# Kernel optimization log

Measured on AMD Instinct MI355X. Metric: run time of the kernel, lower is better.

Reference implementation:

```python
import jax, jax.numpy as jnp
import numpy as np

BS = 4
EMBED = 256
HEADS = 8
LEVELS = 4
POINTS = 4
HD = EMBED // HEADS  # 32
SHAPES = np.array([[96, 96], [48, 48], [24, 24], [12, 12]], dtype=np.int64)
LQ = int((SHAPES[:, 0] * SHAPES[:, 1]).sum())  # 12240


def _offset_bias():
    # faithful to MSDeformableAttention._reset_parameters grid init
    thetas = np.arange(HEADS, dtype=np.float32) * (2.0 * np.pi / HEADS)
    g = np.stack([np.cos(thetas), np.sin(thetas)], -1)
    g = g / np.abs(g).max(-1, keepdims=True)
    g = np.tile(g.reshape(HEADS, 1, 1, 2), (1, LEVELS, POINTS, 1))
    g = g * np.arange(1, POINTS + 1, dtype=np.float32).reshape(1, 1, -1, 1)
    return jnp.asarray(g.reshape(-1), dtype=jnp.float32)


def setup_inputs() -> dict:
    key = jax.random.key(0)
    ks = jax.random.split(key, 8)
    tp = HEADS * LEVELS * POINTS
    d = {}
    d["query"] = jax.random.normal(ks[0], (BS, LQ, EMBED), jnp.float32)
    d["reference_points"] = jax.random.uniform(ks[1], (BS, LQ, LEVELS, 2), jnp.float32)
    d["value"] = jax.random.normal(ks[2], (BS, LQ, EMBED), jnp.float32)
    d["value_spatial_shapes"] = SHAPES  # static numpy, int
    d["W_off"] = jax.random.normal(ks[3], (EMBED, tp * 2), jnp.float32) * 0.01
    d["b_off"] = _offset_bias()
    d["W_attn"] = jax.random.normal(ks[4], (EMBED, tp), jnp.float32) * 0.02
    d["b_attn"] = jnp.zeros((tp,), jnp.float32)
    d["W_val"] = jax.random.normal(ks[5], (EMBED, EMBED), jnp.float32) * (1.0 / np.sqrt(EMBED).astype(np.float32))
    d["b_val"] = jnp.zeros((EMBED,), jnp.float32)
    d["W_out"] = jax.random.normal(ks[6], (EMBED, EMBED), jnp.float32) * (1.0 / np.sqrt(EMBED).astype(np.float32))
    d["b_out"] = jnp.zeros((EMBED,), jnp.float32)
    return d


def _bilinear_sample(img, grid):
    # img: [B,H,W,C]; grid: [B,Q,P,2] in [-1,1] (x,y)
    # matches F.grid_sample(mode='bilinear', padding_mode='zeros', align_corners=False)
    B, H, W, C = img.shape
    gx = (grid[..., 0] + 1.0) * (W * 0.5) - 0.5
    gy = (grid[..., 1] + 1.0) * (H * 0.5) - 0.5
    x0 = jnp.floor(gx)
    y0 = jnp.floor(gy)
    wx = gx - x0
    wy = gy - y0
    x0i = x0.astype(jnp.int32)
    y0i = y0.astype(jnp.int32)
    x1i = x0i + 1
    y1i = y0i + 1
    flat = img.reshape(B, H * W, C)

    def corner(xi, yi, w):
        valid = (xi >= 0) & (xi < W) & (yi >= 0) & (yi < H)
        idx = jnp.clip(yi, 0, H - 1) * W + jnp.clip(xi, 0, W - 1)
        v = jnp.take_along_axis(flat, idx.reshape(B, -1, 1), axis=1)
        v = v.reshape(idx.shape + (C,))
        return v * (w * valid)[..., None]

    return (corner(x0i, y0i, (1.0 - wx) * (1.0 - wy))
            + corner(x1i, y0i, wx * (1.0 - wy))
            + corner(x0i, y1i, (1.0 - wx) * wy)
            + corner(x1i, y1i, wx * wy))


def reference(query, reference_points, value, value_spatial_shapes,
              W_off, b_off, W_attn, b_attn, W_val, b_val, W_out, b_out):
    shapes = np.asarray(value_spatial_shapes)  # static [L,2] (H,W)
    bs, Lq, _ = query.shape
    v = (value @ W_val + b_val).reshape(bs, -1, HEADS, HD)  # [bs,Lv,H,hd]
    off = (query @ W_off + b_off).reshape(bs, Lq, HEADS, LEVELS, POINTS, 2)
    aw = jax.nn.softmax((query @ W_attn + b_attn).reshape(bs, Lq, HEADS, LEVELS * POINTS), axis=-1)
    aw = aw.reshape(bs, Lq, HEADS, LEVELS, POINTS)
    # normalizer is (W,H) per level
    norm = jnp.asarray(shapes[:, ::-1].copy(), jnp.float32).reshape(1, 1, 1, LEVELS, 1, 2)
    loc = reference_points[:, :, None, :, None, :] + off / norm
    grids = 2.0 * loc - 1.0  # [bs,Lq,H,L,P,2]

    acc = jnp.zeros((bs * HEADS, Lq, HD), query.dtype)
    start = 0
    for lvl in range(LEVELS):
        h, w = int(shapes[lvl, 0]), int(shapes[lvl, 1])
        v_l = v[:, start:start + h * w].reshape(bs, h, w, HEADS, HD)
        v_l = v_l.transpose(0, 3, 1, 2, 4).reshape(bs * HEADS, h, w, HD)
        g_l = grids[:, :, :, lvl].transpose(0, 2, 1, 3, 4).reshape(bs * HEADS, Lq, POINTS, 2)
        s_l = _bilinear_sample(v_l, g_l)  # [bs*H, Lq, P, hd]
        w_l = aw[:, :, :, lvl].transpose(0, 2, 1, 3).reshape(bs * HEADS, Lq, POINTS)
        acc = acc + jnp.einsum('bqpc,bqp->bqc', s_l, w_l)
        start += h * w

    out = acc.reshape(bs, HEADS, Lq, HD).transpose(0, 2, 1, 3).reshape(bs, Lq, EMBED)
    return out @ W_out + b_out
```

## Files before the change

### kernel.cpp

```cpp
#include <hip/hip_runtime.h>
#include <hip/hip_bf16.h>

static constexpr int BS     = 4;
static constexpr int EMBED  = 256;
static constexpr int HEADS  = 8;
static constexpr int LEVELS = 4;
static constexpr int POINTS = 4;
static constexpr int HD     = 32;
static constexpr int LQ     = 12240;
static constexpr int NROW   = BS * LQ;
static constexpr int LVL_W[4]  = {96, 48, 24, 12};
static constexpr int LVL_H[4]  = {96, 48, 24, 12};
static constexpr int LVL_ST[4] = {0, 9216, 11520, 12096};

typedef __attribute__((ext_vector_type(8))) short short8;
typedef __attribute__((ext_vector_type(4))) float f32x4;
typedef __attribute__((ext_vector_type(2))) float f32x2;

__device__ __forceinline__ unsigned short f2bf(float f) {
    unsigned int u = __float_as_uint(f);
    unsigned int r = (u + 0x7FFFu + ((u >> 16) & 1u)) >> 16;
    return (unsigned short)r;
}
__device__ __forceinline__ float bf2f(unsigned short b) {
    return __uint_as_float(((unsigned int)b) << 16);
}

__device__ __forceinline__ void pkfma(f32x2& a, unsigned int u, f32x2 w) {
    f32x2 v;
    v.x = __uint_as_float(u << 16);
    v.y = __uint_as_float(u & 0xffff0000u);
    asm("v_pk_fma_f32 %0, %1, %2, %0" : "+v"(a) : "v"(v), "v"(w));
}

__global__ __launch_bounds__(256) void prep_weights(
    const float* __restrict__ W_off, const float* __restrict__ W_attn,
    const float* __restrict__ W_val, const float* __restrict__ W_out,
    unsigned short* __restrict__ WT_oa, unsigned short* __restrict__ WT_val,
    unsigned short* __restrict__ WT_out)
{
    const int gid = blockIdx.x * 256 + threadIdx.x;
    const int k = gid & 255;
    const int n = gid >> 8;
    if (n < 384) {
        const float v = (n < 256) ? W_off[k * 256 + n] : W_attn[k * 128 + (n - 256)];
        WT_oa[n * 256 + k] = f2bf(v);
    } else if (n < 640) {
        const int nn = n - 384;
        WT_val[nn * 256 + k] = f2bf(W_val[k * 256 + nn]);
    } else {
        const int nn = n - 640;
        WT_out[nn * 256 + k] = f2bf(W_out[k * 256 + nn]);
    }
}

template <int NTW, bool A_BF16, bool OUT_BF16>
__global__ __launch_bounds__(256) void gemm_mfma(
    const void* __restrict__ Av, const unsigned short* __restrict__ Wt,
    const float* __restrict__ bias0, const float* __restrict__ bias1, int nsplit,
    void* __restrict__ Cv, int N)
{
    constexpr int NB = NTW * 64;
    constexpr int K  = 256;
    __shared__ __align__(16) unsigned short As[64][40];
    __shared__ __align__(16) unsigned short Bs[NB][40];

    const int tid = threadIdx.x;
    const int m0 = blockIdx.y * 64;
    const int n0 = blockIdx.x * NB;
    const int w  = tid >> 6;
    const int l  = tid & 63;
    const int lm = l & 15;
    const int lq = l >> 4;

    const int sr = tid >> 2;
    const int kg = (tid & 3) * 8;

    float4 pa0, pa1; short8 pa_bf;
    short8 pb[NTW];

    auto gload = [&](int k0) {
        if (A_BF16) {
            const unsigned short* A = (const unsigned short*)Av;
            pa_bf = *(const short8*)&A[(size_t)(m0 + sr) * K + k0 + kg];
        } else {
            const float* A = (const float*)Av;
            const float* ap = &A[(size_t)(m0 + sr) * K + k0 + kg];
            pa0 = *(const float4*)ap;
            pa1 = *(const float4*)(ap + 4);
        }
        #pragma unroll
        for (int i = 0; i < NTW; ++i) {
            const int slot = tid + i * 256;
            const int n  = slot >> 2;
            const int kk = (slot & 3) * 8;
            pb[i] = *(const short8*)&Wt[(size_t)(n0 + n) * K + k0 + kk];
        }
    };

    f32x4 acc[4][NTW];
    #pragma unroll
    for (int rg = 0; rg < 4; ++rg)
        #pragma unroll
        for (int nt = 0; nt < NTW; ++nt)
            acc[rg][nt] = (f32x4){0.f, 0.f, 0.f, 0.f};

    gload(0);
    #pragma unroll 2
    for (int k0 = 0; k0 < K; k0 += 32) {
        if (A_BF16) {
            *(short8*)&As[sr][kg] = pa_bf;
        } else {
            uint4 pk;
            pk.x = (unsigned int)f2bf(pa0.x) | ((unsigned int)f2bf(pa0.y) << 16);
            pk.y = (unsigned int)f2bf(pa0.z) | ((unsigned int)f2bf(pa0.w) << 16);
            pk.z = (unsigned int)f2bf(pa1.x) | ((unsigned int)f2bf(pa1.y) << 16);
            pk.w = (unsigned int)f2bf(pa1.z) | ((unsigned int)f2bf(pa1.w) << 16);
            *(uint4*)&As[sr][kg] = pk;
        }
        #pragma unroll
        for (int i = 0; i < NTW; ++i) {
            const int slot = tid + i * 256;
            const int n  = slot >> 2;
            const int kk = (slot & 3) * 8;
            *(short8*)&Bs[n][kk] = pb[i];
        }
        __syncthreads();

        if (k0 + 32 < K) gload(k0 + 32);

        short8 af[4];
        #pragma unroll
        for (int rg = 0; rg < 4; ++rg)
            af[rg] = *(const short8*)&As[rg * 16 + lm][lq * 8];
        #pragma unroll
        for (int nt = 0; nt < NTW; ++nt) {
            const short8 bf = *(const short8*)&Bs[(w * NTW + nt) * 16 + lm][lq * 8];
            #pragma unroll
            for (int rg = 0; rg < 4; ++rg)
                acc[rg][nt] = __builtin_amdgcn_mfma_f32_16x16x32_bf16(af[rg], bf, acc[rg][nt], 0, 0, 0);
        }
        __syncthreads();
    }

    #pragma unroll
    for (int nt = 0; nt < NTW; ++nt) {
        const int col = n0 + (w * NTW + nt) * 16 + lm;
        const float b = (col < nsplit) ? bias0[col] : bias1[col - nsplit];
        #pragma unroll
        for (int rg = 0; rg < 4; ++rg)
            #pragma unroll
            for (int r = 0; r < 4; ++r) {
                const int row = m0 + rg * 16 + lq * 4 + r;
                const float v = acc[rg][nt][r] + b;
                if (OUT_BF16) ((unsigned short*)Cv)[(size_t)row * N + col] = f2bf(v);
                else          ((float*)Cv)[(size_t)row * N + col] = v;
            }
    }
}

__global__ __launch_bounds__(256) void loc_aw_kernel(
    float* __restrict__ OA, const float* __restrict__ refp)
{
    const int tid = threadIdx.x;
    const int row = blockIdx.x * 2 + (tid >> 7);
    const int t = tid & 127;
    const int l = (t >> 2) & 3;
    float* rowp = OA + (size_t)row * 384;

    float logit = rowp[256 + t];
    float m = logit;
    #pragma unroll
    for (int d = 8; d >= 1; d >>= 1) m = fmaxf(m, __shfl_xor(m, d, 16));
    float e = __expf(logit - m);
    float s = e;
    #pragma unroll
    for (int d = 8; d >= 1; d >>= 1) s += __shfl_xor(s, d, 16);
    rowp[256 + t] = e / s;

    const float ox = rowp[t * 2 + 0];
    const float oy = rowp[t * 2 + 1];
    const float rx = refp[(size_t)row * 8 + l * 2 + 0];
    const float ry = refp[(size_t)row * 8 + l * 2 + 1];
    const float Wl = (float)LVL_W[l];
    const float Hl = (float)LVL_H[l];
    const float lx = rx + ox / Wl;
    const float ly = ry + oy / Hl;
    rowp[t * 2 + 0] = lx * Wl - 0.5f;
    rowp[t * 2 + 1] = ly * Hl - 0.5f;
}

__global__ __launch_bounds__(256) void sample_kernel(
    const unsigned short* __restrict__ V,
    const float* __restrict__ OA,
    unsigned short* __restrict__ ACC)
{
    __shared__ unsigned int pr[512 * 12];

    const int tid = threadIdx.x;

    #pragma unroll
    for (int ss = 0; ss < 2; ++ss) {
        const int s  = tid + ss * 256;
        const int lp = s >> 5;
        const int r  = (s >> 3) & 3;
        const int h  = s & 7;
        const int lvl = lp >> 2;
        const int Wl = LVL_W[lvl], Hl = LVL_H[lvl], st = LVL_ST[lvl];
        const float* rowp = OA + (size_t)(blockIdx.x * 4 + r) * 384;

        const float gx  = rowp[h * 32 + lp * 2 + 0];
        const float gy  = rowp[h * 32 + lp * 2 + 1];
        const float wgt = rowp[256 + h * 16 + lp];

        const float fx = floorf(gx), fy = floorf(gy);
        const float wx = gx - fx,    wy = gy - fy;
        const int x0 = (int)fx, y0 = (int)fy;
        const int x1 = x0 + 1,  y1 = y0 + 1;

        const bool bx0 = ((unsigned)x0 < (unsigned)Wl);
        const bool bx1 = ((unsigned)x1 < (unsigned)Wl);
        const bool by0 = ((unsigned)y0 < (unsigned)Hl);
        const bool by1 = ((unsigned)y1 < (unsigned)Hl);
        const float w00 = (bx0 && by0) ? (1.f - wx) * (1.f - wy) * wgt : 0.f;
        const float w10 = (bx1 && by0) ? wx * (1.f - wy) * wgt : 0.f;
        const float w01 = (bx0 && by1) ? (1.f - wx) * wy * wgt : 0.f;
        const float w11 = (bx1 && by1) ? wx * wy * wgt : 0.f;

        const int cx0 = min(max(x0, 0), Wl - 1);
        const int cx1 = min(max(x1, 0), Wl - 1);
        const int cy0 = min(max(y0, 0), Hl - 1);
        const int cy1 = min(max(y1, 0), Hl - 1);

        unsigned int* p = &pr[s * 12];
        uint4 o;
        o.x = (unsigned int)(st + cy0 * Wl + cx0) * 512u;
        o.y = (unsigned int)(st + cy0 * Wl + cx1) * 512u;
        o.z = (unsigned int)(st + cy1 * Wl + cx0) * 512u;
        o.w = (unsigned int)(st + cy1 * Wl + cx1) * 512u;
        *(uint4*)p = o;
        uint4 wA, wB;
        wA.x = __float_as_uint(w00); wA.y = wA.x;
        wA.z = __float_as_uint(w10); wA.w = wA.z;
        wB.x = __float_as_uint(w01); wB.y = wB.x;
        wB.z = __float_as_uint(w11); wB.w = wB.z;
        *(uint4*)(p + 4) = wA;
        *(uint4*)(p + 8) = wB;
    }
    __syncthreads();

    const int w    = tid >> 6;
    const int l    = tid & 63;
    const int half = l >> 5;
    const int head = (l >> 2) & 7;
    const int c16  = (l & 3) * 16;

    const int row  = __builtin_amdgcn_readfirstlane(blockIdx.x * 4 + w);
    const int b    = row / LQ;
    const char* vrow = (const char*)V + (size_t)b * ((size_t)LQ * 512);
    const unsigned int lane_byte = (unsigned int)(head * 64 + c16);
    const int sid0 = half * 8 * 32 + w * 8 + head;

    unsigned int ofs[2][4];
    f32x2 wp[2][4];
    uint4 dat[2][4];
    f32x2 acc[4];
    #pragma unroll
    for (int i = 0; i < 4; ++i) acc[i] = (f32x2){0.f, 0.f};

    auto ldprep = [&](int j, int buf) {
        const unsigned int* p = &pr[(sid0 + j * 32) * 12];
        const uint4 o = *(const uint4*)p;
        ofs[buf][0] = o.x; ofs[buf][1] = o.y; ofs[buf][2] = o.z; ofs[buf][3] = o.w;
        #pragma unroll
        for (int c = 0; c < 4; ++c)
            wp[buf][c] = *(const f32x2*)(p + 4 + 2 * c);
    };
    auto ldval = [&](int buf) {
        #pragma unroll
        for (int c = 0; c < 4; ++c)
            dat[buf][c] = *(const uint4*)(vrow + (lane_byte + ofs[buf][c]));
    };
    auto consume = [&](int buf) {
        #pragma unroll
        for (int c = 0; c < 4; ++c) {
            const uint4 d = dat[buf][c];
            const f32x2 ww = wp[buf][c];
            pkfma(acc[0], d.x, ww);
            pkfma(acc[1], d.y, ww);
            pkfma(acc[2], d.z, ww);
            pkfma(acc[3], d.w, ww);
        }
    };

    ldprep(0, 0);
    ldval(0);
    #pragma unroll
    for (int j = 0; j < 8; ++j) {
        if (j < 7) {
            ldprep(j + 1, (j + 1) & 1);
            ldval((j + 1) & 1);
        }
        consume(j & 1);
    }

    #pragma unroll
    for (int i = 0; i < 4; ++i) {
        acc[i].x += __shfl_xor(acc[i].x, 32);
        acc[i].y += __shfl_xor(acc[i].y, 32);
    }
    if (half == 0) {
        uint4 o;
        o.x = (unsigned int)f2bf(acc[0].x) | ((unsigned int)f2bf(acc[0].y) << 16);
        o.y = (unsigned int)f2bf(acc[1].x) | ((unsigned int)f2bf(acc[1].y) << 16);
        o.z = (unsigned int)f2bf(acc[2].x) | ((unsigned int)f2bf(acc[2].y) << 16);
        o.w = (unsigned int)f2bf(acc[3].x) | ((unsigned int)f2bf(acc[3].y) << 16);
        *(uint4*)((char*)(ACC + (size_t)row * EMBED) + head * 64 + c16) = o;
    }
}

extern "C" void kernel_launch(void* const* d_in, const int* in_sizes, int n_in,
                              void* d_out, int out_size, void* d_ws, size_t ws_size,
                              hipStream_t stream) {
    const float* query  = (const float*)d_in[0];
    const float* refp   = (const float*)d_in[1];
    const float* value  = (const float*)d_in[2];
    const float* W_off  = (const float*)d_in[4];
    const float* b_off  = (const float*)d_in[5];
    const float* W_attn = (const float*)d_in[6];
    const float* b_attn = (const float*)d_in[7];
    const float* W_val  = (const float*)d_in[8];
    const float* b_val  = (const float*)d_in[9];
    const float* W_out  = (const float*)d_in[10];
    const float* b_out  = (const float*)d_in[11];
    float* out = (float*)d_out;

    unsigned short* WT_oa  = (unsigned short*)d_ws;
    unsigned short* WT_val = WT_oa  + 384 * 256;
    unsigned short* WT_out = WT_val + 256 * 256;
    unsigned short* V      = WT_out + 256 * 256;
    float*          OA     = (float*)(V + (size_t)NROW * EMBED);
    unsigned short* ACCb   = (unsigned short*)(OA + (size_t)NROW * 384);

    dim3 blk(256);

    prep_weights<<<896, blk, 0, stream>>>(W_off, W_attn, W_val, W_out,
                                          WT_oa, WT_val, WT_out);
    gemm_mfma<4, false, true><<<dim3(1, NROW / 64), blk, 0, stream>>>(
        value, WT_val, b_val, b_val, 256, V, 256);
    gemm_mfma<3, false, false><<<dim3(2, NROW / 64), blk, 0, stream>>>(
        query, WT_oa, b_off, b_attn, 256, OA, 384);
    loc_aw_kernel<<<NROW / 2, blk, 0, stream>>>(OA, refp);
    sample_kernel<<<NROW / 4, blk, 0, stream>>>(V, OA, ACCb);
    gemm_mfma<4, true, false><<<dim3(1, NROW / 64), blk, 0, stream>>>(
        ACCb, WT_out, b_out, b_out, 256, out, 256);
}
```

Baseline: 382.9 us.

## Fuse softmax and location computation into the sampling kernel

Removes the separate loc_aw kernel and computes the softmax over attention logits and the sampling coordinates inside the sampling kernel's prep phase, using shared-memory reductions. This avoids a launch and a read-modify-write pass over the 384-column OA buffer. The LDS layout is shrunk from 12 to 8 words per sample by storing four scalar weights instead of duplicated pairs. The inner loop is also restructured to pair corners for packed FMA, with a final horizontal add. The trade-off is extra syncthreads and a reduction inside the sampling kernel, plus a launch-bounds occupancy hint.

```diff
diff --git a/kernel.cpp b/kernel.cpp
--- a/kernel.cpp
+++ b/kernel.cpp
@@ -22,14 +22,8 @@
     unsigned int r = (u + 0x7FFFu + ((u >> 16) & 1u)) >> 16;
     return (unsigned short)r;
 }
-__device__ __forceinline__ float bf2f(unsigned short b) {
-    return __uint_as_float(((unsigned int)b) << 16);
-}
-
-__device__ __forceinline__ void pkfma(f32x2& a, unsigned int u, f32x2 w) {
-    f32x2 v;
-    v.x = __uint_as_float(u << 16);
-    v.y = __uint_as_float(u & 0xffff0000u);
+
+__device__ __forceinline__ void pkfma(f32x2& a, f32x2 v, f32x2 w) {
     asm("v_pk_fma_f32 %0, %1, %2, %0" : "+v"(a) : "v"(v), "v"(w));
 }
 
@@ -159,93 +153,95 @@
     }
 }
 
-__global__ __launch_bounds__(256) void loc_aw_kernel(
-    float* __restrict__ OA, const float* __restrict__ refp)
-{
-    const int tid = threadIdx.x;
-    const int row = blockIdx.x * 2 + (tid >> 7);
-    const int t = tid & 127;
-    const int l = (t >> 2) & 3;
-    float* rowp = OA + (size_t)row * 384;
-
-    float logit = rowp[256 + t];
-    float m = logit;
-    #pragma unroll
-    for (int d = 8; d >= 1; d >>= 1) m = fmaxf(m, __shfl_xor(m, d, 16));
-    float e = __expf(logit - m);
-    float s = e;
-    #pragma unroll
-    for (int d = 8; d >= 1; d >>= 1) s += __shfl_xor(s, d, 16);
-    rowp[256 + t] = e / s;
-
-    const float ox = rowp[t * 2 + 0];
-    const float oy = rowp[t * 2 + 1];
-    const float rx = refp[(size_t)row * 8 + l * 2 + 0];
-    const float ry = refp[(size_t)row * 8 + l * 2 + 1];
-    const float Wl = (float)LVL_W[l];
-    const float Hl = (float)LVL_H[l];
-    const float lx = rx + ox / Wl;
-    const float ly = ry + oy / Hl;
-    rowp[t * 2 + 0] = lx * Wl - 0.5f;
-    rowp[t * 2 + 1] = ly * Hl - 0.5f;
-}
-
-__global__ __launch_bounds__(256) void sample_kernel(
+__global__ __launch_bounds__(256, 8) void sample_kernel(
     const unsigned short* __restrict__ V,
     const float* __restrict__ OA,
+    const float* __restrict__ refp,
     unsigned short* __restrict__ ACC)
 {
-    __shared__ unsigned int pr[512 * 12];
+    __shared__ __align__(16) unsigned int pr_o[512][4];
+    __shared__ __align__(16) unsigned int pr_w[512][4];
 
     const int tid = threadIdx.x;
 
-    #pragma unroll
-    for (int ss = 0; ss < 2; ++ss) {
-        const int s  = tid + ss * 256;
-        const int lp = s >> 5;
-        const int r  = (s >> 3) & 3;
-        const int h  = s & 7;
-        const int lvl = lp >> 2;
-        const int Wl = LVL_W[lvl], Hl = LVL_H[lvl], st = LVL_ST[lvl];
-        const float* rowp = OA + (size_t)(blockIdx.x * 4 + r) * 384;
-
-        const float gx  = rowp[h * 32 + lp * 2 + 0];
-        const float gy  = rowp[h * 32 + lp * 2 + 1];
-        const float wgt = rowp[256 + h * 16 + lp];
-
-        const float fx = floorf(gx), fy = floorf(gy);
-        const float wx = gx - fx,    wy = gy - fy;
-        const int x0 = (int)fx, y0 = (int)fy;
-        const int x1 = x0 + 1,  y1 = y0 + 1;
-
-        const bool bx0 = ((unsigned)x0 < (unsigned)Wl);
-        const bool bx1 = ((unsigned)x1 < (unsigned)Wl);
-        const bool by0 = ((unsigned)y0 < (unsigned)Hl);
-        const bool by1 = ((unsigned)y1 < (unsigned)Hl);
-        const float w00 = (bx0 && by0) ? (1.f - wx) * (1.f - wy) * wgt : 0.f;
-        const float w10 = (bx1 && by0) ? wx * (1.f - wy) * wgt : 0.f;
-        const float w01 = (bx0 && by1) ? (1.f - wx) * wy * wgt : 0.f;
-        const float w11 = (bx1 && by1) ? wx * wy * wgt : 0.f;
-
-        const int cx0 = min(max(x0, 0), Wl - 1);
-        const int cx1 = min(max(x1, 0), Wl - 1);
-        const int cy0 = min(max(y0, 0), Hl - 1);
-        const int cy1 = min(max(y1, 0), Hl - 1);
-
-        unsigned int* p = &pr[s * 12];
-        uint4 o;
-        o.x = (unsigned int)(st + cy0 * Wl + cx0) * 512u;
-        o.y = (unsigned int)(st + cy0 * Wl + cx1) * 512u;
-        o.z = (unsigned int)(st + cy1 * Wl + cx0) * 512u;
-        o.w = (unsigned int)(st + cy1 * Wl + cx1) * 512u;
-        *(uint4*)p = o;
-        uint4 wA, wB;
-        wA.x = __float_as_uint(w00); wA.y = wA.x;
-        wA.z = __float_as_uint(w10); wA.w = wA.z;
-        wB.x = __float_as_uint(w01); wB.y = wB.x;
-        wB.z = __float_as_uint(w11); wB.w = wB.z;
-        *(uint4*)(p + 4) = wA;
-        *(uint4*)(p + 8) = wB;
+    {
+        const int g = tid & 31;
+        const int r = g >> 3;
+        const int h = g & 7;
+        const int L = tid >> 5;
+        const int prow = blockIdx.x * 4 + r;
+        const float* rowp = OA + (size_t)prow * 384;
+
+        const float lg0 = rowp[256 + h * 16 + L];
+        const float lg1 = rowp[256 + h * 16 + L + 8];
+
+        float* smax = (float*)pr_w;
+        float* ssum = smax + 264;
+        smax[L * 33 + g] = fmaxf(lg0, lg1);
+        __syncthreads();
+        float m = smax[g];
+        #pragma unroll
+        for (int k = 1; k < 8; ++k) m = fmaxf(m, smax[k * 33 + g]);
+        const float e0 = __expf(lg0 - m);
+        const float e1 = __expf(lg1 - m);
+        ssum[L * 33 + g] = e0 + e1;
+        __syncthreads();
+        float sden = ssum[g];
+        #pragma unroll
+        for (int k = 1; k < 8; ++k) sden += ssum[k * 33 + g];
+        const float inv = 1.0f / sden;
+
+        uint4 wstash[2];
+        int   sidx[2];
+        #pragma unroll
+        for (int ss = 0; ss < 2; ++ss) {
+            const int lp  = L + ss * 8;
+            const int s   = lp * 32 + g;
+            const int lvl = lp >> 2;
+            const int Wl = LVL_W[lvl], Hl = LVL_H[lvl], st = LVL_ST[lvl];
+
+            const float2 oxy = *(const float2*)&rowp[h * 32 + lp * 2];
+            const float2 rxy = *(const float2*)&refp[(size_t)prow * 8 + lvl * 2];
+            const float wgt = (ss ? e1 : e0) * inv;
+
+            const float gx = (rxy.x + oxy.x / (float)Wl) * (float)Wl - 0.5f;
+            const float gy = (rxy.y + oxy.y / (float)Hl) * (float)Hl - 0.5f;
+
+            const float fx = floorf(gx), fy = floorf(gy);
+            const float wx = gx - fx,    wy = gy - fy;
+            const int x0 = (int)fx, y0 = (int)fy;
+            const int x1 = x0 + 1,  y1 = y0 + 1;
+
+            const bool bx0 = ((unsigned)x0 < (unsigned)Wl);
+            const bool bx1 = ((unsigned)x1 < (unsigned)Wl);
+            const bool by0 = ((unsigned)y0 < (unsigned)Hl);
+            const bool by1 = ((unsigned)y1 < (unsigned)Hl);
+            const float w00 = (bx0 && by0) ? (1.f - wx) * (1.f - wy) * wgt : 0.f;
+            const float w10 = (bx1 && by0) ? wx * (1.f - wy) * wgt : 0.f;
+            const float w01 = (bx0 && by1) ? (1.f - wx) * wy * wgt : 0.f;
+            const float w11 = (bx1 && by1) ? wx * wy * wgt : 0.f;
+
+            const int cx0 = min(max(x0, 0), Wl - 1);
+            const int cx1 = min(max(x1, 0), Wl - 1);
+            const int cy0 = min(max(y0, 0), Hl - 1);
+            const int cy1 = min(max(y1, 0), Hl - 1);
+
+            uint4 o;
+            o.x = (unsigned int)(st + cy0 * Wl + cx0) * 512u;
+            o.y = (unsigned int)(st + cy0 * Wl + cx1) * 512u;
+            o.z = (unsigned int)(st + cy1 * Wl + cx0) * 512u;
+            o.w = (unsigned int)(st + cy1 * Wl + cx1) * 512u;
+            *(uint4*)&pr_o[s][0] = o;
+
+            uint4 wv;
+            wv.x = __float_as_uint(w00); wv.y = __float_as_uint(w10);
+            wv.z = __float_as_uint(w01); wv.w = __float_as_uint(w11);
+            wstash[ss] = wv;
+            sidx[ss] = s;
+        }
+        __syncthreads();
+        *(uint4*)&pr_w[sidx[0]][0] = wstash[0];
+        *(uint4*)&pr_w[sidx[1]][0] = wstash[1];
     }
     __syncthreads();
 
@@ -259,62 +255,67 @@
     const int b    = row / LQ;
     const char* vrow = (const char*)V + (size_t)b * ((size_t)LQ * 512);
     const unsigned int lane_byte = (unsigned int)(head * 64 + c16);
-    const int sid0 = half * 8 * 32 + w * 8 + head;
-
-    unsigned int ofs[2][4];
-    f32x2 wp[2][4];
+    const int sid0 = half * 256 + w * 8 + head;
+
     uint4 dat[2][4];
-    f32x2 acc[4];
-    #pragma unroll
-    for (int i = 0; i < 4; ++i) acc[i] = (f32x2){0.f, 0.f};
-
-    auto ldprep = [&](int j, int buf) {
-        const unsigned int* p = &pr[(sid0 + j * 32) * 12];
-        const uint4 o = *(const uint4*)p;
-        ofs[buf][0] = o.x; ofs[buf][1] = o.y; ofs[buf][2] = o.z; ofs[buf][3] = o.w;
-        #pragma unroll
-        for (int c = 0; c < 4; ++c)
-            wp[buf][c] = *(const f32x2*)(p + 4 + 2 * c);
+    f32x2 accA[4], accB[4];
+    #pragma unroll
+    for (int i = 0; i < 4; ++i) { accA[i] = (f32x2){0.f,0.f}; accB[i] = (f32x2){0.f,0.f}; }
+
+    auto ldissue = [&](int j, int buf) {
+        const uint4 o = *(const uint4*)&pr_o[sid0 + j * 32][0];
+        dat[buf][0] = *(const uint4*)(vrow + (lane_byte + o.x));
+        dat[buf][1] = *(const uint4*)(vrow + (lane_byte + o.y));
+        dat[buf][2] = *(const uint4*)(vrow + (lane_byte + o.z));
+        dat[buf][3] = *(const uint4*)(vrow + (lane_byte + o.w));
     };
-    auto ldval = [&](int buf) {
-        #pragma unroll
-        for (int c = 0; c < 4; ++c)
-            dat[buf][c] = *(const uint4*)(vrow + (lane_byte + ofs[buf][c]));
+    auto pkstep = [&](f32x2& A, f32x2& B, unsigned u0, unsigned u1, f32x2 w2) {
+        f32x2 pa, pb;
+        pa.x = __uint_as_float(u0 << 16);
+        pa.y = __uint_as_float(u1 << 16);
+        pb.x = __uint_as_float(u0 & 0xffff0000u);
+        pb.y = __uint_as_float(u1 & 0xffff0000u);
+        pkfma(A, pa, w2);
+        pkfma(B, pb, w2);
     };
-    auto consume = [&](int buf) {
-        #pragma unroll
-        for (int c = 0; c < 4; ++c) {
-            const uint4 d = dat[buf][c];
-            const f32x2 ww = wp[buf][c];
-            pkfma(acc[0], d.x, ww);
-            pkfma(acc[1], d.y, ww);
-            pkfma(acc[2], d.z, ww);
-            pkfma(acc[3], d.w, ww);
-        }
+    auto consume = [&](int j, int buf) {
+        const f32x4 wv = *(const f32x4*)&pr_w[sid0 + j * 32][0];
+        f32x2 w01; w01.x = wv.x; w01.y = wv.y;
+        f32x2 w23; w23.x = wv.z; w23.y = wv.w;
+        const uint4 d0 = dat[buf][0], d1 = dat[buf][1];
+        pkstep(accA[0], accB[0], d0.x, d1.x, w01);
+        pkstep(accA[1], accB[1], d0.y, d1.y, w01);
+        pkstep(accA[2], accB[2], d0.z, d1.z, w01);
+        pkstep(accA[3], accB[3], d0.w, d1.w, w01);
+        const uint4 d2 = dat[buf][2], d3 = dat[buf][3];
+        pkstep(accA[0], accB[0], d2.x, d3.x, w23);
+        pkstep(accA[1], accB[1], d2.y, d3.y, w23);
+        pkstep(accA[2], accB[2], d2.z, d3.z, w23);
+        pkstep(accA[3], accB[3], d2.w, d3.w, w23);
     };
 
-    ldprep(0, 0);
-    ldval(0);
+    ldissue(0, 0);
     #pragma unroll
     for (int j = 0; j < 8; ++j) {
-        if (j < 7) {
-            ldprep(j + 1, (j + 1) & 1);
-            ldval((j + 1) & 1);
-        }
-        consume(j & 1);
-    }
-
+        if (j < 7) ldissue(j + 1, (j + 1) & 1);
+        consume(j, j & 1);
+    }
+
+    float c[8];
     #pragma unroll
     for (int i = 0; i < 4; ++i) {
-        acc[i].x += __shfl_xor(acc[i].x, 32);
-        acc[i].y += __shfl_xor(acc[i].y, 32);
-    }
+        c[2 * i]     = accA[i].x + accA[i].y;
+        c[2 * i + 1] = accB[i].x + accB[i].y;
+    }
+    #pragma unroll
+    for (int i = 0; i < 8; ++i) c[i] += __shfl_xor(c[i], 32);
+
     if (half == 0) {
         uint4 o;
-        o.x = (unsigned int)f2bf(acc[0].x) | ((unsigned int)f2bf(acc[0].y) << 16);
-        o.y = (unsigned int)f2bf(acc[1].x) | ((unsigned int)f2bf(acc[1].y) << 16);
-        o.z = (unsigned int)f2bf(acc[2].x) | ((unsigned int)f2bf(acc[2].y) << 16);
-        o.w = (unsigned int)f2bf(acc[3].x) | ((unsigned int)f2bf(acc[3].y) << 16);
+        o.x = (unsigned int)f2bf(c[0]) | ((unsigned int)f2bf(c[1]) << 16);
+        o.y = (unsigned int)f2bf(c[2]) | ((unsigned int)f2bf(c[3]) << 16);
+        o.z = (unsigned int)f2bf(c[4]) | ((unsigned int)f2bf(c[5]) << 16);
+        o.w = (unsigned int)f2bf(c[6]) | ((unsigned int)f2bf(c[7]) << 16);
         *(uint4*)((char*)(ACC + (size_t)row * EMBED) + head * 64 + c16) = o;
     }
 }
@@ -350,8 +351,7 @@
         value, WT_val, b_val, b_val, 256, V, 256);
     gemm_mfma<3, false, false><<<dim3(2, NROW / 64), blk, 0, stream>>>(
         query, WT_oa, b_off, b_attn, 256, OA, 384);
-    loc_aw_kernel<<<NROW / 2, blk, 0, stream>>>(OA, refp);
-    sample_kernel<<<NROW / 4, blk, 0, stream>>>(V, OA, ACCb);
+    sample_kernel<<<NROW / 4, blk, 0, stream>>>(V, OA, refp, ACCb);
     gemm_mfma<4, true, false><<<dim3(1, NROW / 64), blk, 0, stream>>>(
         ACCb, WT_out, b_out, b_out, 256, out, 256);
 }
```

New measurement: 368.3 us. 3.8% less time.
